# Optimization experiments

Measured on AMD Instinct MI355X. Metric: run time of the kernel, lower is better.

The kernel has to match this reference:

```python
import jax, jax.numpy as jnp
import numpy as np

B, S, DIM = 1, 2048, 4096
NH, NKV, HD = 32, 8, 128
REPEATS = NH // NKV
ROPE_THETA = 10000.0


def setup_inputs() -> dict:
    key = jax.random.key(0)
    ks = jax.random.split(key, 6)
    x = jax.random.normal(ks[0], (B, S, DIM), jnp.float32) * 0.02
    wq = jax.random.normal(ks[1], (NH * HD, DIM), jnp.float32) * 0.02
    wk = jax.random.normal(ks[2], (NKV * HD, DIM), jnp.float32) * 0.02
    wv = jax.random.normal(ks[3], (NKV * HD, DIM), jnp.float32) * 0.02
    wo = jax.random.normal(ks[4], (DIM, NH * HD), jnp.float32) * 0.02
    # rotary frequencies (real cos/sin form of complex freqs_cis)
    inv_freq = 1.0 / (ROPE_THETA ** (jnp.arange(0, HD, 2, dtype=jnp.float32) / HD))
    ang = jnp.arange(S, dtype=jnp.float32)[:, None] * inv_freq[None, :]  # [S, HD//2]
    freqs_cos = jnp.cos(ang)
    freqs_sin = jnp.sin(ang)
    positions = jnp.arange(S, dtype=jnp.int32)  # prompt phase: all positions
    # additive causal mask
    mask = jnp.where(jnp.tril(jnp.ones((S, S), bool)), 0.0, -1e9).astype(jnp.float32)
    cache_k = jnp.zeros((B, S, NKV, HD), jnp.float32)
    cache_v = jnp.zeros((B, S, NKV, HD), jnp.float32)
    return dict(x=x, wq=wq, wk=wk, wv=wv, wo=wo, freqs_cos=freqs_cos,
                freqs_sin=freqs_sin, cache_k=cache_k, cache_v=cache_v,
                positions=positions, mask=mask)


def apply_rope(t, cos, sin):
    # t: [b, s, h, d]; pairs are (d0,d1),(d2,d3),... matching view_as_complex
    tr = t[..., 0::2]
    ti = t[..., 1::2]
    c = cos[None, :, None, :]
    s = sin[None, :, None, :]
    out_r = tr * c - ti * s
    out_i = tr * s + ti * c
    return jnp.stack([out_r, out_i], axis=-1).reshape(t.shape)


def reference(x, wq, wk, wv, wo, freqs_cos, freqs_sin, cache_k, cache_v, positions, mask):
    b, s, _ = x.shape
    xq = jnp.einsum('bsd,od->bso', x, wq).reshape(b, s, NH, HD)
    xk = jnp.einsum('bsd,od->bso', x, wk).reshape(b, s, NKV, HD)
    xv = jnp.einsum('bsd,od->bso', x, wv).reshape(b, s, NKV, HD)
    xq = apply_rope(xq, freqs_cos, freqs_sin)
    xk = apply_rope(xk, freqs_cos, freqs_sin)
    # KV-cache scatter (prompt phase writes; output uses fresh xk/xv here)
    cache_k = cache_k.at[:, positions].set(xk)
    cache_v = cache_v.at[:, positions].set(xv)
    # GQA: repeat_interleave kv heads to match query heads
    k = jnp.repeat(xk, REPEATS, axis=2).transpose(0, 2, 1, 3)  # [b, NH, s, HD]
    v = jnp.repeat(xv, REPEATS, axis=2).transpose(0, 2, 1, 3)
    q = xq.transpose(0, 2, 1, 3)
    scale = HD ** -0.5
    scores = jnp.einsum('bhqd,bhkd->bhqk', q, k) * scale + mask[None, None]
    probs = jax.nn.softmax(scores.astype(jnp.float32), axis=-1).astype(q.dtype)
    out = jnp.einsum('bhqk,bhkd->bhqd', probs, v)
    out = out.transpose(0, 2, 1, 3).reshape(b, s, NH * HD)
    return jnp.einsum('bso,do->bsd', out, wo)
```

## Files before the change

### kernel.cpp

```cpp
#include <hip/hip_runtime.h>
#include <hip/hip_bf16.h>
#include <stdint.h>

typedef __bf16 bf16_t;
typedef __attribute__((ext_vector_type(8))) __bf16 bf16x8;
typedef __attribute__((ext_vector_type(4))) float f32x4;
typedef __attribute__((ext_vector_type(8))) unsigned short u16x8;

#define S_LEN 2048
#define DIM   4096
#define QKVN  6144
#define NHEAD 32
#define HDIM  128

typedef __attribute__((address_space(1))) unsigned int as1_u32;
typedef __attribute__((address_space(3))) unsigned int as3_u32;

__device__ __forceinline__ unsigned short f2bf(float f) {
  unsigned u = __builtin_bit_cast(unsigned, f);
  u += 0x7fffu + ((u >> 16) & 1u);
  return (unsigned short)(u >> 16);
}

__device__ __forceinline__ void gload_lds16(const void* g, void* l) {
  __builtin_amdgcn_global_load_lds(
      (as1_u32*)(unsigned long long)(uintptr_t)g,
      (as3_u32*)(unsigned int)(uintptr_t)l,
      16, 0, 0);
}

__global__ __launch_bounds__(256) void cvt5_kernel(const float* __restrict__ x,
                                                   const float* __restrict__ wq,
                                                   const float* __restrict__ wk,
                                                   const float* __restrict__ wv,
                                                   const float* __restrict__ wo,
                                                   ushort4* __restrict__ xb,
                                                   ushort4* __restrict__ wqkvb,
                                                   ushort4* __restrict__ wob) {
  const long N0 = 2097152;
  const long N1 = N0 + 4194304;
  const long N2 = N1 + 1048576;
  const long N3 = N2 + 1048576;
  const long N4 = N3 + 4194304;
  long idx = (long)blockIdx.x * 256 + threadIdx.x;
  long stride = (long)gridDim.x * 256;
  for (long i = idx; i < N4; i += stride) {
    const float4* s; ushort4* d; long o;
    if (i < N0)      { s = (const float4*)x;  d = xb;              o = i; }
    else if (i < N1) { s = (const float4*)wq; d = wqkvb;           o = i - N0; }
    else if (i < N2) { s = (const float4*)wk; d = wqkvb + 4194304; o = i - N1; }
    else if (i < N3) { s = (const float4*)wv; d = wqkvb + 5242880; o = i - N2; }
    else             { s = (const float4*)wo; d = wob;             o = i - N3; }
    float4 v = s[o];
    ushort4 r;
    r.x = f2bf(v.x); r.y = f2bf(v.y); r.z = f2bf(v.z); r.w = f2bf(v.w);
    d[o] = r;
  }
}

__device__ __forceinline__ bf16x8 fld(const char* half, int row, int chunk) {
  return *(const bf16x8*)(half + row * 128 + ((chunk ^ (row & 7)) << 4));
}

__device__ __forceinline__ void mfma8(const bf16x8 (*af)[2], const bf16x8 (*bf_)[2],
                                      f32x4 (*acc)[4], int mbase, int nbase) {
#pragma unroll
  for (int m = 0; m < 4; ++m)
#pragma unroll
    for (int n = 0; n < 2; ++n) {
      acc[mbase + m][nbase + n] = __builtin_amdgcn_mfma_f32_16x16x32_bf16(
          af[mbase + m][0], bf_[nbase + n][0], acc[mbase + m][nbase + n], 0, 0, 0);
      acc[mbase + m][nbase + n] = __builtin_amdgcn_mfma_f32_16x16x32_bf16(
          af[mbase + m][1], bf_[nbase + n][1], acc[mbase + m][nbase + n], 0, 0, 0);
    }
}

template <int OUTF32>
__global__ __launch_bounds__(512, 2) void gemm8p(const bf16_t* __restrict__ A,
                                                 const bf16_t* __restrict__ B,
                                                 void* __restrict__ Cout,
                                                 int M, int N, int K, int nxt) {
  __shared__ char lds[131072];
  const int tid = threadIdx.x;
  const int lane = tid & 63, w = tid >> 6;
  const int wm = w >> 2, wn = w & 3;
  const int lg = lane >> 4, lr = lane & 15;
  const int nwg = gridDim.x;
  const int orig = blockIdx.x;
  const int wgid = (orig & 7) * (nwg >> 3) + (orig >> 3);
  const int bx = wgid % nxt, by = wgid / nxt;
  const long rowA = (long)by * 256;
  const long rowB = (long)bx * 256;

  f32x4 acc[8][4];
  const f32x4 z4 = {0.f, 0.f, 0.f, 0.f};
#pragma unroll
  for (int i = 0; i < 8; ++i)
#pragma unroll
    for (int j = 0; j < 4; ++j) acc[i][j] = z4;

  const int r0 = tid >> 3, sl = tid & 7;
  const long xo  = (long)((sl ^ (r0 & 7)) << 3);
  const long aof = (rowA + r0) * (long)K + xo;
  const long bof = (rowB + r0) * (long)K + xo;
  const long j1  = (long)64 * K;
  const long h1  = (long)128 * K;
  const int ld0 = tid * 16, ld1 = (tid + 512) * 16;

#define STG_A(K0, HALF, DBUF)                                                  \
  { char* hp = lds + (DBUF) * 65536 + (HALF) * 16384;                          \
    gload_lds16(A + aof + (HALF) * h1 + (K0),      hp + ld0);                  \
    gload_lds16(A + aof + (HALF) * h1 + j1 + (K0), hp + ld1); }
#define STG_B(K0, HALF, DBUF)                                                  \
  { char* hp = lds + (DBUF) * 65536 + 32768 + (HALF) * 16384;                  \
    gload_lds16(B + bof + (HALF) * h1 + (K0),      hp + ld0);                  \
    gload_lds16(B + bof + (HALF) * h1 + j1 + (K0), hp + ld1); }

  const int nt = K >> 6;
  const int bro = (wn & 1) * 64;

  STG_A(0, 0, 0); STG_A(0, 1, 0); STG_B(0, 0, 0); STG_B(0, 1, 0);
  STG_B(64, 0, 1); STG_B(64, 1, 1);
  asm volatile("s_waitcnt vmcnt(4)" ::: "memory");
  __builtin_amdgcn_s_barrier();

  bf16x8 af[8][2], bf_[4][2];

  for (int t = 0; t < nt; ++t) {
    const int d = t & 1;
    const char* Ah = lds + d * 65536 + wm * 16384;
    const char* Bh = lds + d * 65536 + 32768 + (wn >> 1) * 16384;
    const int k1 = (t + 1) << 6, k2 = (t + 2) << 6;
#pragma unroll
    for (int m = 0; m < 4; ++m) {
      af[m][0] = fld(Ah, m * 16 + lr, lg);
      af[m][1] = fld(Ah, m * 16 + lr, 4 + lg);
    }
#pragma unroll
    for (int n = 0; n < 2; ++n) {
      bf_[n][0] = fld(Bh, bro + n * 16 + lr, lg);
      bf_[n][1] = fld(Bh, bro + n * 16 + lr, 4 + lg);
    }
    if (t + 1 < nt) STG_A(k1, 0, d ^ 1);
    __builtin_amdgcn_s_barrier();
    asm volatile("s_waitcnt lgkmcnt(0)" ::: "memory");
    __builtin_amdgcn_sched_barrier(0);
    __builtin_amdgcn_s_setprio(1);
    mfma8(af, bf_, acc, 0, 0);
    __builtin_amdgcn_s_setprio(0);
    __builtin_amdgcn_s_barrier();
#pragma unroll
    for (int n = 2; n < 4; ++n) {
      bf_[n][0] = fld(Bh, bro + n * 16 + lr, lg);
      bf_[n][1] = fld(Bh, bro + n * 16 + lr, 4 + lg);
    }
    if (t + 1 < nt) STG_A(k1, 1, d ^ 1);
    __builtin_amdgcn_s_barrier();
    asm volatile("s_waitcnt lgkmcnt(0)" ::: "memory");
    __builtin_amdgcn_sched_barrier(0);
    __builtin_amdgcn_s_setprio(1);
    mfma8(af, bf_, acc, 0, 2);
    __builtin_amdgcn_s_setprio(0);
    __builtin_amdgcn_s_barrier();
#pragma unroll
    for (int m = 4; m < 8; ++m) {
      af[m][0] = fld(Ah, m * 16 + lr, lg);
      af[m][1] = fld(Ah, m * 16 + lr, 4 + lg);
    }
    if (t + 2 < nt) STG_B(k2, 0, d);
    __builtin_amdgcn_s_barrier();
    asm volatile("s_waitcnt lgkmcnt(0)" ::: "memory");
    __builtin_amdgcn_sched_barrier(0);
    __builtin_amdgcn_s_setprio(1);
    mfma8(af, bf_, acc, 4, 0);
    __builtin_amdgcn_s_setprio(0);
    __builtin_amdgcn_s_barrier();
    if (t + 2 < nt) STG_B(k2, 1, d);
    __builtin_amdgcn_s_barrier();
    __builtin_amdgcn_s_setprio(1);
    mfma8(af, bf_, acc, 4, 2);
    __builtin_amdgcn_s_setprio(0);
    if (t + 2 < nt) {
      asm volatile("s_waitcnt vmcnt(4)" ::: "memory");
    } else {
      asm volatile("s_waitcnt vmcnt(0)" ::: "memory");
    }
    __builtin_amdgcn_s_barrier();
  }
#undef STG_A
#undef STG_B

  const long crow = rowA + wm * 128;
  const long ccol = rowB + wn * 64;
  if (OUTF32) {
    float* C = (float*)Cout;
#pragma unroll
    for (int mf = 0; mf < 8; ++mf)
#pragma unroll
      for (int j = 0; j < 4; ++j) {
        long row = crow + mf * 16 + lg * 4 + j;
        float* cp = C + row * N + ccol + lr;
#pragma unroll
        for (int nf = 0; nf < 4; ++nf) cp[nf * 16] = acc[mf][nf][j];
      }
  } else {
    unsigned short* C = (unsigned short*)Cout;
#pragma unroll
    for (int mf = 0; mf < 8; ++mf)
#pragma unroll
      for (int j = 0; j < 4; ++j) {
        long row = crow + mf * 16 + lg * 4 + j;
        unsigned short* cp = C + row * N + ccol + lr;
#pragma unroll
        for (int nf = 0; nf < 4; ++nf) cp[nf * 16] = f2bf(acc[mf][nf][j]);
      }
  }
}

template <int OUTF32>
__global__ __launch_bounds__(512, 2) void gemm8r(const bf16_t* __restrict__ A,
                                                 const bf16_t* __restrict__ B,
                                                 void* __restrict__ Cout,
                                                 int M, int N, int K, int nxt) {
  __shared__ char lds[98304];
  const int tid = threadIdx.x;
  const int lane = tid & 63, w = tid >> 6;
  const int wm = w >> 1, wn = w & 1;
  const int lg = lane >> 4, lr = lane & 15;
  const int nwg = gridDim.x;
  const int orig = blockIdx.x;
  const int wgid = (orig & 7) * (nwg >> 3) + (orig >> 3);
  const int bx = wgid % nxt, by = wgid / nxt;
  const long rowA = (long)by * 256;
  const long rowB = (long)bx * 128;

  f32x4 acc[4][4];
  const f32x4 z4 = {0.f, 0.f, 0.f, 0.f};
#pragma unroll
  for (int i = 0; i < 4; ++i)
#pragma unroll
    for (int j = 0; j < 4; ++j) acc[i][j] = z4;

  const int r0 = tid >> 3, sl = tid & 7;
  const long xo  = (long)((sl ^ (r0 & 7)) << 3);
  const long aof = (rowA + r0) * (long)K + xo;
  const long bof = (rowB + r0) * (long)K + xo;
  const long r64 = (long)64 * K;
  const int ld0 = tid * 16, ld1 = (tid + 512) * 16;

#define RSTG_A(K0, HALF, DBUF)                                                 \
  { char* ap = lds + (DBUF) * 49152 + (HALF) * 16384;                          \
    gload_lds16(A + aof + (HALF) * 2 * r64 + (K0),       ap + ld0);            \
    gload_lds16(A + aof + (HALF) * 2 * r64 + r64 + (K0), ap + ld1); }
#define RSTG_B(K0, DBUF)                                                       \
  { char* bp = lds + (DBUF) * 49152 + 32768;                                   \
    gload_lds16(B + bof + (K0),       bp + ld0);                               \
    gload_lds16(B + bof + r64 + (K0), bp + ld1); }

  const int nt = K >> 6;

  RSTG_A(0, 0, 0); RSTG_A(0, 1, 0); RSTG_B(0, 0);
  RSTG_B(64, 1);
  asm volatile("s_waitcnt vmcnt(2)" ::: "memory");
  __builtin_amdgcn_s_barrier();

  bf16x8 af[4][2], bf_[4][2];

  for (int t = 0; t < nt; ++t) {
    const int d = t & 1;
    const char* Ar = lds + d * 49152;
    const char* Br = Ar + 32768;
    const int arow = wm * 64, brow = wn * 64;
    const int k1 = (t + 1) << 6, k2 = (t + 2) << 6;
#pragma unroll
    for (int m = 0; m < 2; ++m) {
      af[m][0] = fld(Ar, arow + m * 16 + lr, lg);
      af[m][1] = fld(Ar, arow + m * 16 + lr, 4 + lg);
    }
#pragma unroll
    for (int n = 0; n < 2; ++n) {
      bf_[n][0] = fld(Br, brow + n * 16 + lr, lg);
      bf_[n][1] = fld(Br, brow + n * 16 + lr, 4 + lg);
    }
    if (t + 1 < nt) RSTG_A(k1, 0, d ^ 1);
    __builtin_amdgcn_s_barrier();
    asm volatile("s_waitcnt lgkmcnt(0)" ::: "memory");
    __builtin_amdgcn_sched_barrier(0);
    __builtin_amdgcn_s_setprio(1);
#pragma unroll
    for (int m = 0; m < 2; ++m)
#pragma unroll
      for (int n = 0; n < 2; ++n) {
        acc[m][n] = __builtin_amdgcn_mfma_f32_16x16x32_bf16(af[m][0], bf_[n][0], acc[m][n], 0, 0, 0);
        acc[m][n] = __builtin_amdgcn_mfma_f32_16x16x32_bf16(af[m][1], bf_[n][1], acc[m][n], 0, 0, 0);
      }
    __builtin_amdgcn_s_setprio(0);
    __builtin_amdgcn_s_barrier();
#pragma unroll
    for (int n = 2; n < 4; ++n) {
      bf_[n][0] = fld(Br, brow + n * 16 + lr, lg);
      bf_[n][1] = fld(Br, brow + n * 16 + lr, 4 + lg);
    }
    if (t + 1 < nt) RSTG_A(k1, 1, d ^ 1);
    __builtin_amdgcn_s_barrier();
    asm volatile("s_waitcnt lgkmcnt(0)" ::: "memory");
    __builtin_amdgcn_sched_barrier(0);
    __builtin_amdgcn_s_setprio(1);
#pragma unroll
    for (int m = 0; m < 2; ++m)
#pragma unroll
      for (int n = 2; n < 4; ++n) {
        acc[m][n] = __builtin_amdgcn_mfma_f32_16x16x32_bf16(af[m][0], bf_[n][0], acc[m][n], 0, 0, 0);
        acc[m][n] = __builtin_amdgcn_mfma_f32_16x16x32_bf16(af[m][1], bf_[n][1], acc[m][n], 0, 0, 0);
      }
    __builtin_amdgcn_s_setprio(0);
    __builtin_amdgcn_s_barrier();
#pragma unroll
    for (int m = 2; m < 4; ++m) {
      af[m][0] = fld(Ar, arow + m * 16 + lr, lg);
      af[m][1] = fld(Ar, arow + m * 16 + lr, 4 + lg);
    }
    if (t + 2 < nt) RSTG_B(k2, d);
    __builtin_amdgcn_s_barrier();
    asm volatile("s_waitcnt lgkmcnt(0)" ::: "memory");
    __builtin_amdgcn_sched_barrier(0);
    __builtin_amdgcn_s_setprio(1);
#pragma unroll
    for (int m = 2; m < 4; ++m)
#pragma unroll
      for (int n = 0; n < 2; ++n) {
        acc[m][n] = __builtin_amdgcn_mfma_f32_16x16x32_bf16(af[m][0], bf_[n][0], acc[m][n], 0, 0, 0);
        acc[m][n] = __builtin_amdgcn_mfma_f32_16x16x32_bf16(af[m][1], bf_[n][1], acc[m][n], 0, 0, 0);
      }
    __builtin_amdgcn_s_setprio(0);
    __builtin_amdgcn_s_barrier();
    __builtin_amdgcn_s_setprio(1);
#pragma unroll
    for (int m = 2; m < 4; ++m)
#pragma unroll
      for (int n = 2; n < 4; ++n) {
        acc[m][n] = __builtin_amdgcn_mfma_f32_16x16x32_bf16(af[m][0], bf_[n][0], acc[m][n], 0, 0, 0);
        acc[m][n] = __builtin_amdgcn_mfma_f32_16x16x32_bf16(af[m][1], bf_[n][1], acc[m][n], 0, 0, 0);
      }
    __builtin_amdgcn_s_setprio(0);
    if (t + 2 < nt) {
      asm volatile("s_waitcnt vmcnt(2)" ::: "memory");
    } else {
      asm volatile("s_waitcnt vmcnt(0)" ::: "memory");
    }
    __builtin_amdgcn_s_barrier();
  }
#undef RSTG_A
#undef RSTG_B

  const long crow = rowA + wm * 64;
  const long ccol = rowB + wn * 64;
  if (OUTF32) {
    float* C = (float*)Cout;
#pragma unroll
    for (int mf = 0; mf < 4; ++mf)
#pragma unroll
      for (int j = 0; j < 4; ++j) {
        long row = crow + mf * 16 + lg * 4 + j;
        float* cp = C + row * N + ccol + lr;
#pragma unroll
        for (int nf = 0; nf < 4; ++nf) cp[nf * 16] = acc[mf][nf][j];
      }
  } else {
    unsigned short* C = (unsigned short*)Cout;
#pragma unroll
    for (int mf = 0; mf < 4; ++mf)
#pragma unroll
      for (int j = 0; j < 4; ++j) {
        long row = crow + mf * 16 + lg * 4 + j;
        unsigned short* cp = C + row * N + ccol + lr;
#pragma unroll
        for (int nf = 0; nf < 4; ++nf) cp[nf * 16] = f2bf(acc[mf][nf][j]);
      }
  }
}

__global__ __launch_bounds__(256) void rope_kernel(unsigned int* __restrict__ qkv32,
                                                   const float* __restrict__ cosb,
                                                   const float* __restrict__ sinb) {
  int t = blockIdx.x * 256 + threadIdx.x;
  int i  = t & 63;
  int sh = t >> 6;
  int hh = sh % 40;
  int s  = sh / 40;
  int col2 = (hh < 32) ? (hh * 64 + i) : (2048 + (hh - 32) * 64 + i);
  unsigned int* p = qkv32 + (long)s * (QKVN / 2) + col2;
  unsigned int v = *p;
  float tr = __builtin_bit_cast(float, (v & 0xffffu) << 16);
  float ti = __builtin_bit_cast(float, v & 0xffff0000u);
  float c  = cosb[s * 64 + i];
  float sn = sinb[s * 64 + i];
  float orr = tr * c - ti * sn;
  float oi  = tr * sn + ti * c;
  *p = (unsigned int)f2bf(orr) | ((unsigned int)f2bf(oi) << 16);
}

__global__ __launch_bounds__(256) void vtrans_kernel(const bf16_t* __restrict__ qkv,
                                                     bf16_t* __restrict__ vT) {
  const int kh = blockIdx.x;
  const int hd = threadIdx.x & 127;
  const int s0 = blockIdx.y * 16 + (threadIdx.x >> 7) * 8;
  u16x8 v;
#pragma unroll
  for (int e = 0; e < 8; ++e)
    v[e] = *(const unsigned short*)(qkv + (long)(s0 + e) * QKVN + 5120 + kh * HDIM + hd);
  *(u16x8*)(vT + ((long)kh * HDIM + hd) * S_LEN + s0) = v;
}

__global__ __launch_bounds__(512) void attn_kernel(const bf16_t* __restrict__ qkv,
                                                   const bf16_t* __restrict__ vT,
                                                   unsigned short* __restrict__ ob) {
  __shared__ bf16_t Kt[64 * 128];
  __shared__ bf16_t Vt[128 * 64];
  __shared__ bf16_t Pl[8 * 16 * 64];
  const int h  = blockIdx.x;
  const int qi = 15 - (int)blockIdx.y;
  const int qb = qi * 128;
  const int kh = h >> 2;
  const int tid = threadIdx.x, lane = tid & 63, w = tid >> 6;
  const int lg = lane >> 4, lr = lane & 15;
  const int qrow0 = qb + w * 16;

  bf16x8 qf[4];
  const bf16_t* qptr = qkv + (long)(qrow0 + lr) * QKVN + h * HDIM + lg * 8;
#pragma unroll
  for (int kk = 0; kk < 4; ++kk) qf[kk] = *(const bf16x8*)(qptr + kk * 32);

  const f32x4 z4 = {0.f, 0.f, 0.f, 0.f};
  f32x4 oacc[8];
#pragma unroll
  for (int c = 0; c < 8; ++c) oacc[c] = z4;
  float m[4]    = {-1e30f, -1e30f, -1e30f, -1e30f};
  float lsum[4] = {0.f, 0.f, 0.f, 0.f};

  char* KtB = (char*)Kt;
  char* VtB = (char*)Vt;
  char* PlB = (char*)Pl + w * 2048;
  const float scale = 0.08838834764831845f;
  const int ntiles = 2 * qi + 2;
  const int wqmax = qrow0 + 15;

  for (int t = 0; t < ntiles; ++t) {
    const int kv0 = t * 64;
    __syncthreads();
#pragma unroll
    for (int it = 0; it < 2; ++it) {
      int cch = tid + it * 512;
      int r = cch >> 4, c = cch & 15;
      const bf16_t* src = qkv + (long)(kv0 + r) * QKVN + 4096 + kh * HDIM
                          + ((c ^ (r & 7)) * 8);
      gload_lds16(src, KtB + cch * 16);
    }
#pragma unroll
    for (int it = 0; it < 2; ++it) {
      int cch = tid + it * 512;
      int hd = cch >> 3, c = cch & 7;
      const bf16_t* src = vT + ((long)kh * HDIM + hd) * S_LEN + kv0
                          + ((c ^ (hd & 7)) * 8);
      gload_lds16(src, VtB + cch * 16);
    }
    __syncthreads();
    if (kv0 > wqmax) continue;

    f32x4 sf[4];
#pragma unroll
    for (int f = 0; f < 4; ++f) {
      f32x4 a = z4;
      int n = f * 16 + lr;
      int rb = n * 256, sw = (n & 7) << 4;
#pragma unroll
      for (int kk = 0; kk < 4; ++kk) {
        bf16x8 kf = *(const bf16x8*)(KtB + rb + (((kk * 4 + lg) * 16) ^ sw));
        a = __builtin_amdgcn_mfma_f32_16x16x32_bf16(qf[kk], kf, a, 0, 0, 0);
      }
      sf[f] = a;
    }

    float sc_arr[4];
#pragma unroll
    for (int j = 0; j < 4; ++j) {
      int qrow = qrow0 + lg * 4 + j;
      float sv[4];
#pragma unroll
      for (int f = 0; f < 4; ++f) {
        float s = sf[f][j] * scale;
        if (kv0 + f * 16 + lr > qrow) s = -1e9f;
        sv[f] = s;
      }
      float mx = fmaxf(fmaxf(sv[0], sv[1]), fmaxf(sv[2], sv[3]));
      mx = fmaxf(mx, __shfl_xor(mx, 1));
      mx = fmaxf(mx, __shfl_xor(mx, 2));
      mx = fmaxf(mx, __shfl_xor(mx, 4));
      mx = fmaxf(mx, __shfl_xor(mx, 8));
      float mn = fmaxf(m[j], mx);
      float p[4];
#pragma unroll
      for (int f = 0; f < 4; ++f) p[f] = __expf(sv[f] - mn);
      float ps = (p[0] + p[1]) + (p[2] + p[3]);
      ps += __shfl_xor(ps, 1);
      ps += __shfl_xor(ps, 2);
      ps += __shfl_xor(ps, 4);
      ps += __shfl_xor(ps, 8);
      float sc = __expf(m[j] - mn);
      lsum[j] = lsum[j] * sc + ps;
      m[j] = mn;
      sc_arr[j] = sc;
      int row = lg * 4 + j;
      int swp = (row & 7) << 4;
#pragma unroll
      for (int f = 0; f < 4; ++f)
        *(unsigned short*)(PlB + row * 128 + (((f * 16 + lr) * 2) ^ swp)) = f2bf(p[f]);
    }
#pragma unroll
    for (int c = 0; c < 8; ++c)
#pragma unroll
      for (int j = 0; j < 4; ++j) oacc[c][j] *= sc_arr[j];

    bf16x8 pfr[2];
#pragma unroll
    for (int kk = 0; kk < 2; ++kk)
      pfr[kk] = *(const bf16x8*)(PlB + lr * 128 + (((kk * 4 + lg) * 16) ^ ((lr & 7) << 4)));
#pragma unroll
    for (int c = 0; c < 8; ++c) {
      int hd = c * 16 + lr;
      int rb = hd * 128, sw = (hd & 7) << 4;
#pragma unroll
      for (int kk = 0; kk < 2; ++kk) {
        bf16x8 vf = *(const bf16x8*)(VtB + rb + (((kk * 4 + lg) * 16) ^ sw));
        oacc[c] = __builtin_amdgcn_mfma_f32_16x16x32_bf16(pfr[kk], vf, oacc[c], 0, 0, 0);
      }
    }
  }

  float rl[4];
#pragma unroll
  for (int j = 0; j < 4; ++j) rl[j] = 1.f / lsum[j];
#pragma unroll
  for (int c = 0; c < 8; ++c)
#pragma unroll
    for (int j = 0; j < 4; ++j) {
      long row = qrow0 + lg * 4 + j;
      ob[row * 4096 + h * 128 + c * 16 + lr] = f2bf(oacc[c][j] * rl[j]);
    }
}

extern "C" void kernel_launch(void* const* d_in, const int* in_sizes, int n_in,
                              void* d_out, int out_size, void* d_ws, size_t ws_size,
                              hipStream_t stream) {
  const float* x  = (const float*)d_in[0];
  const float* wq = (const float*)d_in[1];
  const float* wk = (const float*)d_in[2];
  const float* wv = (const float*)d_in[3];
  const float* wo = (const float*)d_in[4];
  const float* fc = (const float*)d_in[5];
  const float* fs = (const float*)d_in[6];

  char* ws = (char*)d_ws;
  bf16_t* xb    = (bf16_t*)(ws + 0);
  bf16_t* wqkvb = (bf16_t*)(ws + 16777216);
  bf16_t* wob   = (bf16_t*)(ws + 67108864);
  bf16_t* qkv   = (bf16_t*)(ws + 100663296);
  bf16_t* ob    = (bf16_t*)(ws + 125829120);
  bf16_t* vT    = (bf16_t*)(ws + 0);

  cvt5_kernel<<<2048, 256, 0, stream>>>(x, wq, wk, wv, wo,
                                        (ushort4*)xb, (ushort4*)wqkvb, (ushort4*)wob);

  gemm8p<0><<<192, 512, 0, stream>>>(xb, wqkvb, qkv, 2048, 6144, 4096, 24);
  vtrans_kernel<<<dim3(8, 128), 256, 0, stream>>>(qkv, vT);
  rope_kernel<<<20480, 256, 0, stream>>>((unsigned int*)qkv, fc, fs);
  attn_kernel<<<dim3(32, 16), 512, 0, stream>>>(qkv, vT, (unsigned short*)ob);
  gemm8r<1><<<256, 512, 0, stream>>>(ob, wob, d_out, 2048, 4096, 4096, 32);
}
```

Measured before the change: 330.1 us.

## Retile QKV GEMM to 256x192 tiles so the grid fills all CUs

```diff
diff --git a/kernel.cpp b/kernel.cpp
--- a/kernel.cpp
+++ b/kernel.cpp
@@ -62,25 +62,12 @@
   return *(const bf16x8*)(half + row * 128 + ((chunk ^ (row & 7)) << 4));
 }
 
-__device__ __forceinline__ void mfma8(const bf16x8 (*af)[2], const bf16x8 (*bf_)[2],
-                                      f32x4 (*acc)[4], int mbase, int nbase) {
-#pragma unroll
-  for (int m = 0; m < 4; ++m)
-#pragma unroll
-    for (int n = 0; n < 2; ++n) {
-      acc[mbase + m][nbase + n] = __builtin_amdgcn_mfma_f32_16x16x32_bf16(
-          af[mbase + m][0], bf_[nbase + n][0], acc[mbase + m][nbase + n], 0, 0, 0);
-      acc[mbase + m][nbase + n] = __builtin_amdgcn_mfma_f32_16x16x32_bf16(
-          af[mbase + m][1], bf_[nbase + n][1], acc[mbase + m][nbase + n], 0, 0, 0);
-    }
-}
-
 template <int OUTF32>
-__global__ __launch_bounds__(512, 2) void gemm8p(const bf16_t* __restrict__ A,
+__global__ __launch_bounds__(512, 2) void gemm8q(const bf16_t* __restrict__ A,
                                                  const bf16_t* __restrict__ B,
                                                  void* __restrict__ Cout,
                                                  int M, int N, int K, int nxt) {
-  __shared__ char lds[131072];
+  __shared__ char lds[114688];
   const int tid = threadIdx.x;
   const int lane = tid & 63, w = tid >> 6;
   const int wm = w >> 2, wn = w & 3;
@@ -90,14 +77,14 @@
   const int wgid = (orig & 7) * (nwg >> 3) + (orig >> 3);
   const int bx = wgid % nxt, by = wgid / nxt;
   const long rowA = (long)by * 256;
-  const long rowB = (long)bx * 256;
-
-  f32x4 acc[8][4];
+  const long rowB = (long)bx * 192;
+
+  f32x4 acc[8][3];
   const f32x4 z4 = {0.f, 0.f, 0.f, 0.f};
 #pragma unroll
   for (int i = 0; i < 8; ++i)
 #pragma unroll
-    for (int j = 0; j < 4; ++j) acc[i][j] = z4;
+    for (int j = 0; j < 3; ++j) acc[i][j] = z4;
 
   const int r0 = tid >> 3, sl = tid & 7;
   const long xo  = (long)((sl ^ (r0 & 7)) << 3);
@@ -105,93 +92,124 @@
   const long bof = (rowB + r0) * (long)K + xo;
   const long j1  = (long)64 * K;
   const long h1  = (long)128 * K;
-  const int ld0 = tid * 16, ld1 = (tid + 512) * 16;
-
-#define STG_A(K0, HALF, DBUF)                                                  \
-  { char* hp = lds + (DBUF) * 65536 + (HALF) * 16384;                          \
+  const int ld0 = tid * 16, ld1 = (tid + 512) * 16, ld2 = (tid + 1024) * 16;
+
+#define QSTG_A(K0, HALF, DBUF)                                                 \
+  { char* hp = lds + (DBUF) * 57344 + (HALF) * 16384;                          \
     gload_lds16(A + aof + (HALF) * h1 + (K0),      hp + ld0);                  \
     gload_lds16(A + aof + (HALF) * h1 + j1 + (K0), hp + ld1); }
-#define STG_B(K0, HALF, DBUF)                                                  \
-  { char* hp = lds + (DBUF) * 65536 + 32768 + (HALF) * 16384;                  \
-    gload_lds16(B + bof + (HALF) * h1 + (K0),      hp + ld0);                  \
-    gload_lds16(B + bof + (HALF) * h1 + j1 + (K0), hp + ld1); }
+#define QSTG_B(K0, DBUF)                                                       \
+  { char* bp = lds + (DBUF) * 57344 + 32768;                                   \
+    gload_lds16(B + bof + (K0),          bp + ld0);                            \
+    gload_lds16(B + bof + j1 + (K0),     bp + ld1);                            \
+    gload_lds16(B + bof + 2 * j1 + (K0), bp + ld2); }
 
   const int nt = K >> 6;
-  const int bro = (wn & 1) * 64;
-
-  STG_A(0, 0, 0); STG_A(0, 1, 0); STG_B(0, 0, 0); STG_B(0, 1, 0);
-  STG_B(64, 0, 1); STG_B(64, 1, 1);
-  asm volatile("s_waitcnt vmcnt(4)" ::: "memory");
+  const int brow = wn * 48;
+
+  QSTG_A(0, 0, 0); QSTG_A(0, 1, 0); QSTG_B(0, 0);
+  QSTG_B(64, 1);
+  asm volatile("s_waitcnt vmcnt(3)" ::: "memory");
   __builtin_amdgcn_s_barrier();
 
-  bf16x8 af[8][2], bf_[4][2];
+  bf16x8 af[8][2], bf_[3][2];
 
   for (int t = 0; t < nt; ++t) {
     const int d = t & 1;
-    const char* Ah = lds + d * 65536 + wm * 16384;
-    const char* Bh = lds + d * 65536 + 32768 + (wn >> 1) * 16384;
+    const char* Ah = lds + d * 57344 + wm * 16384;
+    const char* Br = lds + d * 57344 + 32768;
     const int k1 = (t + 1) << 6, k2 = (t + 2) << 6;
 #pragma unroll
-    for (int m = 0; m < 4; ++m) {
+    for (int m = 0; m < 2; ++m) {
       af[m][0] = fld(Ah, m * 16 + lr, lg);
       af[m][1] = fld(Ah, m * 16 + lr, 4 + lg);
     }
 #pragma unroll
-    for (int n = 0; n < 2; ++n) {
-      bf_[n][0] = fld(Bh, bro + n * 16 + lr, lg);
-      bf_[n][1] = fld(Bh, bro + n * 16 + lr, 4 + lg);
-    }
-    if (t + 1 < nt) STG_A(k1, 0, d ^ 1);
-    __builtin_amdgcn_s_barrier();
-    asm volatile("s_waitcnt lgkmcnt(0)" ::: "memory");
-    __builtin_amdgcn_sched_barrier(0);
-    __builtin_amdgcn_s_setprio(1);
-    mfma8(af, bf_, acc, 0, 0);
-    __builtin_amdgcn_s_setprio(0);
-    __builtin_amdgcn_s_barrier();
-#pragma unroll
-    for (int n = 2; n < 4; ++n) {
-      bf_[n][0] = fld(Bh, bro + n * 16 + lr, lg);
-      bf_[n][1] = fld(Bh, bro + n * 16 + lr, 4 + lg);
-    }
-    if (t + 1 < nt) STG_A(k1, 1, d ^ 1);
-    __builtin_amdgcn_s_barrier();
-    asm volatile("s_waitcnt lgkmcnt(0)" ::: "memory");
-    __builtin_amdgcn_sched_barrier(0);
-    __builtin_amdgcn_s_setprio(1);
-    mfma8(af, bf_, acc, 0, 2);
-    __builtin_amdgcn_s_setprio(0);
-    __builtin_amdgcn_s_barrier();
-#pragma unroll
-    for (int m = 4; m < 8; ++m) {
+    for (int n = 0; n < 3; ++n) {
+      bf_[n][0] = fld(Br, brow + n * 16 + lr, lg);
+      bf_[n][1] = fld(Br, brow + n * 16 + lr, 4 + lg);
+    }
+    if (t + 1 < nt) QSTG_A(k1, 0, d ^ 1);
+    __builtin_amdgcn_s_barrier();
+    asm volatile("s_waitcnt lgkmcnt(0)" ::: "memory");
+    __builtin_amdgcn_sched_barrier(0);
+    __builtin_amdgcn_s_setprio(1);
+#pragma unroll
+    for (int m = 0; m < 2; ++m)
+#pragma unroll
+      for (int n = 0; n < 3; ++n) {
+        acc[m][n] = __builtin_amdgcn_mfma_f32_16x16x32_bf16(af[m][0], bf_[n][0], acc[m][n], 0, 0, 0);
+        acc[m][n] = __builtin_amdgcn_mfma_f32_16x16x32_bf16(af[m][1], bf_[n][1], acc[m][n], 0, 0, 0);
+      }
+    __builtin_amdgcn_s_setprio(0);
+    __builtin_amdgcn_s_barrier();
+#pragma unroll
+    for (int m = 2; m < 4; ++m) {
       af[m][0] = fld(Ah, m * 16 + lr, lg);
       af[m][1] = fld(Ah, m * 16 + lr, 4 + lg);
     }
-    if (t + 2 < nt) STG_B(k2, 0, d);
-    __builtin_amdgcn_s_barrier();
-    asm volatile("s_waitcnt lgkmcnt(0)" ::: "memory");
-    __builtin_amdgcn_sched_barrier(0);
-    __builtin_amdgcn_s_setprio(1);
-    mfma8(af, bf_, acc, 4, 0);
-    __builtin_amdgcn_s_setprio(0);
-    __builtin_amdgcn_s_barrier();
-    if (t + 2 < nt) STG_B(k2, 1, d);
-    __builtin_amdgcn_s_barrier();
-    __builtin_amdgcn_s_setprio(1);
-    mfma8(af, bf_, acc, 4, 2);
+    if (t + 1 < nt) QSTG_A(k1, 1, d ^ 1);
+    __builtin_amdgcn_s_barrier();
+    asm volatile("s_waitcnt lgkmcnt(0)" ::: "memory");
+    __builtin_amdgcn_sched_barrier(0);
+    __builtin_amdgcn_s_setprio(1);
+#pragma unroll
+    for (int m = 2; m < 4; ++m)
+#pragma unroll
+      for (int n = 0; n < 3; ++n) {
+        acc[m][n] = __builtin_amdgcn_mfma_f32_16x16x32_bf16(af[m][0], bf_[n][0], acc[m][n], 0, 0, 0);
+        acc[m][n] = __builtin_amdgcn_mfma_f32_16x16x32_bf16(af[m][1], bf_[n][1], acc[m][n], 0, 0, 0);
+      }
+    __builtin_amdgcn_s_setprio(0);
+    __builtin_amdgcn_s_barrier();
+#pragma unroll
+    for (int m = 4; m < 6; ++m) {
+      af[m][0] = fld(Ah, m * 16 + lr, lg);
+      af[m][1] = fld(Ah, m * 16 + lr, 4 + lg);
+    }
+    if (t + 2 < nt) QSTG_B(k2, d);
+    __builtin_amdgcn_s_barrier();
+    asm volatile("s_waitcnt lgkmcnt(0)" ::: "memory");
+    __builtin_amdgcn_sched_barrier(0);
+    __builtin_amdgcn_s_setprio(1);
+#pragma unroll
+    for (int m = 4; m < 6; ++m)
+#pragma unroll
+      for (int n = 0; n < 3; ++n) {
+        acc[m][n] = __builtin_amdgcn_mfma_f32_16x16x32_bf16(af[m][0], bf_[n][0], acc[m][n], 0, 0, 0);
+        acc[m][n] = __builtin_amdgcn_mfma_f32_16x16x32_bf16(af[m][1], bf_[n][1], acc[m][n], 0, 0, 0);
+      }
+    __builtin_amdgcn_s_setprio(0);
+    __builtin_amdgcn_s_barrier();
+#pragma unroll
+    for (int m = 6; m < 8; ++m) {
+      af[m][0] = fld(Ah, m * 16 + lr, lg);
+      af[m][1] = fld(Ah, m * 16 + lr, 4 + lg);
+    }
+    __builtin_amdgcn_s_barrier();
+    asm volatile("s_waitcnt lgkmcnt(0)" ::: "memory");
+    __builtin_amdgcn_sched_barrier(0);
+    __builtin_amdgcn_s_setprio(1);
+#pragma unroll
+    for (int m = 6; m < 8; ++m)
+#pragma unroll
+      for (int n = 0; n < 3; ++n) {
+        acc[m][n] = __builtin_amdgcn_mfma_f32_16x16x32_bf16(af[m][0], bf_[n][0], acc[m][n], 0, 0, 0);
+        acc[m][n] = __builtin_amdgcn_mfma_f32_16x16x32_bf16(af[m][1], bf_[n][1], acc[m][n], 0, 0, 0);
+      }
     __builtin_amdgcn_s_setprio(0);
     if (t + 2 < nt) {
-      asm volatile("s_waitcnt vmcnt(4)" ::: "memory");
+      asm volatile("s_waitcnt vmcnt(3)" ::: "memory");
     } else {
       asm volatile("s_waitcnt vmcnt(0)" ::: "memory");
     }
     __builtin_amdgcn_s_barrier();
   }
-#undef STG_A
-#undef STG_B
+#undef QSTG_A
+#undef QSTG_B
 
   const long crow = rowA + wm * 128;
-  const long ccol = rowB + wn * 64;
+  const long ccol = rowB + wn * 48;
   if (OUTF32) {
     float* C = (float*)Cout;
 #pragma unroll
@@ -201,7 +219,7 @@
         long row = crow + mf * 16 + lg * 4 + j;
         float* cp = C + row * N + ccol + lr;
 #pragma unroll
-        for (int nf = 0; nf < 4; ++nf) cp[nf * 16] = acc[mf][nf][j];
+        for (int nf = 0; nf < 3; ++nf) cp[nf * 16] = acc[mf][nf][j];
       }
   } else {
     unsigned short* C = (unsigned short*)Cout;
@@ -212,7 +230,7 @@
         long row = crow + mf * 16 + lg * 4 + j;
         unsigned short* cp = C + row * N + ccol + lr;
 #pragma unroll
-        for (int nf = 0; nf < 4; ++nf) cp[nf * 16] = f2bf(acc[mf][nf][j]);
+        for (int nf = 0; nf < 3; ++nf) cp[nf * 16] = f2bf(acc[mf][nf][j]);
       }
   }
 }
@@ -571,7 +589,7 @@
   cvt5_kernel<<<2048, 256, 0, stream>>>(x, wq, wk, wv, wo,
                                         (ushort4*)xb, (ushort4*)wqkvb, (ushort4*)wob);
 
-  gemm8p<0><<<192, 512, 0, stream>>>(xb, wqkvb, qkv, 2048, 6144, 4096, 24);
+  gemm8q<0><<<256, 512, 0, stream>>>(xb, wqkvb, qkv, 2048, 6144, 4096, 32);
   vtrans_kernel<<<dim3(8, 128), 256, 0, stream>>>(qkv, vT);
   rope_kernel<<<20480, 256, 0, stream>>>((unsigned int*)qkv, fc, fs);
   attn_kernel<<<dim3(32, 16), 512, 0, stream>>>(qkv, vT, (unsigned short*)ob);
```

Result: no change. 324.4 us (-1.7%).
